# Kernel tuning notes

Hardware: AMD Instinct MI355X
Metric: run time of the kernel (lower is better)

The kernel has to match this reference:

```python
import jax, jax.numpy as jnp
import numpy as np

EMBED_DIM = 1024
HEADS = 16
D_HEAD = EMBED_DIM // HEADS
B, S = 2, 2048


def setup_inputs() -> dict:
    key = jax.random.key(0)
    ks = jax.random.split(key, 7)
    scale = 1.0 / np.sqrt(EMBED_DIM)
    inp = {
        "key": jax.random.normal(ks[0], (B, S, EMBED_DIM), dtype=jnp.float32),
        "query": jax.random.normal(ks[1], (B, S, EMBED_DIM), dtype=jnp.float32),
        "value": jax.random.normal(ks[2], (B, S, EMBED_DIM), dtype=jnp.float32),
        # causal mask, broadcastable to [B, H, Sq, Sk]
        "mask": jnp.tril(jnp.ones((S, S), dtype=bool))[None, None, :, :],
        # torch nn.Linear weights: [out_features, in_features], applied as x @ W.T
        "Wq": jax.random.normal(ks[3], (EMBED_DIM, EMBED_DIM), dtype=jnp.float32) * scale,
        "Wk": jax.random.normal(ks[4], (EMBED_DIM, EMBED_DIM), dtype=jnp.float32) * scale,
        "Wv": jax.random.normal(ks[5], (EMBED_DIM, EMBED_DIM), dtype=jnp.float32) * scale,
        "Wo": jax.random.normal(ks[6], (EMBED_DIM, EMBED_DIM), dtype=jnp.float32) * scale,
    }
    return inp


def reference(key, query, value, mask, Wq, Wk, Wv, Wo):
    b, sq, _ = query.shape
    sk = key.shape[1]
    # projections (torch Linear: x @ W.T), reshape to [B, H, S, Dh]
    q = (query @ Wq.T).reshape(b, sq, HEADS, D_HEAD).transpose(0, 2, 1, 3)
    k = (key @ Wk.T).reshape(b, sk, HEADS, D_HEAD).transpose(0, 2, 1, 3)
    v = (value @ Wv.T).reshape(b, sk, HEADS, D_HEAD).transpose(0, 2, 1, 3)
    # scaled dot-product scores [B, H, Sq, Sk]
    scores = jnp.einsum("bhqd,bhkd->bhqk", q, k) / jnp.sqrt(jnp.float32(D_HEAD))
    scores = jnp.where(mask, scores, jnp.float32(-1e9))
    attn = jax.nn.softmax(scores, axis=-1)
    # dropout p=0.0 -> identity
    out = jnp.einsum("bhqk,bhkd->bhqd", attn, v)  # [B, H, Sq, Dh]
    out = out.transpose(0, 2, 1, 3).reshape(b, sq, EMBED_DIM)
    return out @ Wo.T
```

## Files before the change

kernel.cpp:

```cpp
#include <hip/hip_runtime.h>
#include <stdint.h>


typedef unsigned short ushort_t;
typedef __attribute__((ext_vector_type(8))) __bf16 bf16x8;
typedef __attribute__((ext_vector_type(4))) float floatx4;

#define EMBED 1024
#define SEQ   2048
#define NH    16
#define DH    64
#define QK_SCALE 0.18033688011112042f

__device__ inline ushort_t f2b(float x) {
  unsigned u = __float_as_uint(x);
  u += 0x7FFFu + ((u >> 16) & 1u);
  return (ushort_t)(u >> 16);
}

__device__ inline unsigned pk2(float a, float b) {
  unsigned ua = __float_as_uint(a) + 0x8000u;
  unsigned ub = __float_as_uint(b) + 0x8000u;
  return __builtin_amdgcn_perm(ub, ua, 0x07060302u);
}

__device__ inline void gl_lds16(const ushort_t* g, ushort_t* l) {
  __builtin_amdgcn_global_load_lds(
      (const __attribute__((address_space(1))) unsigned int*)g,
      (__attribute__((address_space(3))) unsigned int*)l, 16, 0, 0);
}

struct CvtArgs {
  const float* src[16];
  ushort_t*    dst[16];
  float        scale[16];
};

__global__ __launch_bounds__(256) void cvt_kernel(CvtArgs a) {
  const int chunk = blockIdx.x >> 9;
  const int off = ((blockIdx.x & 511) << 11) + (threadIdx.x << 3);
  const float sc = a.scale[chunk];
  const float4* s = (const float4*)(a.src[chunk] + off);
  float4 f0 = s[0], f1 = s[1];
  union { ushort_t u[8]; uint4 v; } o;
  o.u[0] = f2b(f0.x * sc); o.u[1] = f2b(f0.y * sc);
  o.u[2] = f2b(f0.z * sc); o.u[3] = f2b(f0.w * sc);
  o.u[4] = f2b(f1.x * sc); o.u[5] = f2b(f1.y * sc);
  o.u[6] = f2b(f1.z * sc); o.u[7] = f2b(f1.w * sc);
  *(uint4*)(a.dst[chunk] + off) = o.v;
}

__device__ inline void store_sub(char* __restrict__ Cv, const int mode,
                                 const int ldc, const int row, const int col,
                                 const floatx4& acc) {
  if (mode == 0) {
    ushort_t* C = (ushort_t*)Cv;
#pragma unroll
    for (int r = 0; r < 4; ++r)
      C[(size_t)(row + r) * ldc + col] = f2b(acc[r]);
  } else if (mode == 1) {
    float* C = (float*)Cv;
#pragma unroll
    for (int r = 0; r < 4; ++r)
      C[(size_t)(row + r) * ldc + col] = acc[r];
  } else {
    ushort_t* C = (ushort_t*)Cv;
    const int b = row >> 11, s = row & 2047;
    const int h = col >> 6, d = col & 63;
    uint2 pk;
    pk.x = pk2(acc[0], acc[1]);
    pk.y = pk2(acc[2], acc[3]);
    *(uint2*)&C[(size_t)((b * NH + h) * DH + d) * SEQ + s] = pk;
  }
}

__device__ inline void gemm512_core(const ushort_t* __restrict__ A,
                                    const ushort_t* __restrict__ W,
                                    char* __restrict__ Cv, const int mode,
                                    const int ldc, const int m0, const int n0) {
  __shared__ ushort_t As[32 * 512];
  __shared__ ushort_t Bs[16 * 512];
  const int tid  = threadIdx.x;
  const int lane = tid & 63;
  const int wid  = tid >> 6;
  const int lm   = lane & 15;
  const int quad = lane >> 4;
  const int wm   = wid >> 1;
  const int wn   = wid & 1;

  floatx4 zero = {0.f, 0.f, 0.f, 0.f};
  floatx4 acc[4][4];
#pragma unroll
  for (int i = 0; i < 4; ++i)
#pragma unroll
    for (int j = 0; j < 4; ++j) acc[i][j] = zero;

  for (int k0 = 0; k0 < EMBED; k0 += 64) {
    __syncthreads();
#pragma unroll
    for (int u = 0; u < 6; ++u) {
      const int c   = wid * 6 + u;
      const int cb  = c & 31;
      const int sub = cb >> 1;
      const int kc  = (cb & 1) * 32 + quad * 8;
      if (c < 32)
        gl_lds16(A + (size_t)(m0 + sub * 16 + lm) * EMBED + k0 + kc, &As[cb * 512]);
      else
        gl_lds16(W + (size_t)(n0 + sub * 16 + lm) * EMBED + k0 + kc, &Bs[cb * 512]);
    }
    __syncthreads();

#pragma unroll
    for (int ks = 0; ks < 2; ++ks) {
      bf16x8 a[4], b[4];
#pragma unroll
      for (int i = 0; i < 4; ++i)
        a[i] = *(const bf16x8*)&As[((wm * 4 + i) * 2 + ks) * 512 + lane * 8];
#pragma unroll
      for (int j = 0; j < 4; ++j)
        b[j] = *(const bf16x8*)&Bs[((wn * 4 + j) * 2 + ks) * 512 + lane * 8];
#pragma unroll
      for (int i = 0; i < 4; ++i)
#pragma unroll
        for (int j = 0; j < 4; ++j)
          acc[i][j] = __builtin_amdgcn_mfma_f32_16x16x32_bf16(a[i], b[j], acc[i][j], 0, 0, 0);
    }
  }

#pragma unroll
  for (int i = 0; i < 4; ++i) {
    const int row = m0 + wm * 64 + i * 16 + quad * 4;
#pragma unroll
    for (int j = 0; j < 4; ++j)
      store_sub(Cv, mode, ldc, row, n0 + wn * 64 + j * 16 + lm, acc[i][j]);
  }
}

struct QkvArgs {
  const ushort_t* A[3];
  const ushort_t* W[3];
  char*           C[3];
};

__global__ __launch_bounds__(512, 4) void qkv_gemm(QkvArgs q) {
  const int z = blockIdx.z;
  gemm512_core(q.A[z], q.W[z], q.C[z], z == 2 ? 2 : 0, EMBED,
               blockIdx.x * 256, blockIdx.y * 128);
}

__global__ __launch_bounds__(256) void o_gemm(const ushort_t* __restrict__ A,
                                              const ushort_t* __restrict__ W,
                                              float* __restrict__ C) {
  __shared__ ushort_t As[16 * 512];
  __shared__ ushort_t Bs[16 * 512];
  const int m0 = blockIdx.x * 128, n0 = blockIdx.y * 128;
  const int tid  = threadIdx.x;
  const int lane = tid & 63;
  const int wid  = tid >> 6;
  const int lm   = lane & 15;
  const int quad = lane >> 4;

  floatx4 zero = {0.f, 0.f, 0.f, 0.f};
  floatx4 acc[4][4];
#pragma unroll
  for (int i = 0; i < 4; ++i)
#pragma unroll
    for (int j = 0; j < 4; ++j) acc[i][j] = zero;

  const int tm = (wid >> 1) * 4;
  const int tn = (wid & 1) * 4;

  for (int k0 = 0; k0 < EMBED; k0 += 64) {
    __syncthreads();
#pragma unroll
    for (int u = 0; u < 8; ++u) {
      const int c   = wid * 8 + u;
      const int cb  = c & 15;
      const int sub = cb >> 1;
      const int kc  = (cb & 1) * 32 + quad * 8;
      if (c < 16)
        gl_lds16(A + (size_t)(m0 + sub * 16 + lm) * EMBED + k0 + kc, &As[cb * 512]);
      else
        gl_lds16(W + (size_t)(n0 + sub * 16 + lm) * EMBED + k0 + kc, &Bs[cb * 512]);
    }
    __syncthreads();

#pragma unroll
    for (int ks = 0; ks < 2; ++ks) {
      bf16x8 a[4], b[4];
#pragma unroll
      for (int i = 0; i < 4; ++i)
        a[i] = *(const bf16x8*)&As[((tm + i) * 2 + ks) * 512 + lane * 8];
#pragma unroll
      for (int j = 0; j < 4; ++j)
        b[j] = *(const bf16x8*)&Bs[((tn + j) * 2 + ks) * 512 + lane * 8];
#pragma unroll
      for (int i = 0; i < 4; ++i)
#pragma unroll
        for (int j = 0; j < 4; ++j)
          acc[i][j] = __builtin_amdgcn_mfma_f32_16x16x32_bf16(a[i], b[j], acc[i][j], 0, 0, 0);
    }
  }

#pragma unroll
  for (int i = 0; i < 4; ++i) {
    const int row = m0 + (wid >> 1) * 64 + i * 16 + quad * 4;
#pragma unroll
    for (int j = 0; j < 4; ++j) {
      const int col = n0 + (wid & 1) * 64 + j * 16 + lm;
#pragma unroll
      for (int r = 0; r < 4; ++r)
        C[(size_t)(row + r) * EMBED + col] = acc[i][j][r];
    }
  }
}

__global__ __launch_bounds__(256) void attn_kernel(const ushort_t* __restrict__ Qp,
                                                   const ushort_t* __restrict__ Kp,
                                                   const ushort_t* __restrict__ VpT,
                                                   ushort_t* __restrict__ Ob) {
  __shared__ ushort_t Qs[16 * 512];
  __shared__ ushort_t Ks[8 * 512];
  __shared__ ushort_t VTs[8 * 512];
  __shared__ ushort_t Pw[4 * 2048];
  const int L = blockIdx.x;
  const int qb = 15 - (L >> 5);
  const int bh = L & 31;
  const int h = bh & (NH - 1), b = bh >> 4;
  const int tid = threadIdx.x, lane = tid & 63, wid = tid >> 6;
  const int lm = lane & 15, quad = lane >> 4;
  const size_t qkbase = ((size_t)b * SEQ) * EMBED + h * DH;
  const size_t vtbase = ((size_t)(b * NH + h)) * DH * SEQ;
  ushort_t* pwb = &Pw[wid * 2048];

#pragma unroll
  for (int u = 0; u < 4; ++u) {
    const int c = wid * 4 + u;
    gl_lds16(Qp + qkbase + (size_t)(qb * 128 + (c >> 1) * 16 + lm) * EMBED
                 + (c & 1) * 32 + quad * 8,
             &Qs[c * 512]);
  }
  asm volatile("s_waitcnt vmcnt(0)" ::: "memory");
  bf16x8 qf[2][2];
#pragma unroll
  for (int qg = 0; qg < 2; ++qg)
#pragma unroll
    for (int ks = 0; ks < 2; ++ks)
      qf[qg][ks] = *(const bf16x8*)&Qs[((wid * 2 + qg) * 2 + ks) * 512 + lane * 8];

  float l_part[2] = {0.f, 0.f};
  floatx4 zero = {0.f, 0.f, 0.f, 0.f};
  floatx4 o_acc[4][2];
#pragma unroll
  for (int d = 0; d < 4; ++d)
#pragma unroll
    for (int qg = 0; qg < 2; ++qg) o_acc[d][qg] = zero;

  const int kt_end = 2 * qb + 1;
  for (int kt = 0; kt <= kt_end; ++kt) {
    __syncthreads();
#pragma unroll
    for (int u = 0; u < 4; ++u) {
      const int t = wid * 4 + u;
      const int cb = t & 7;
      const int sub = cb >> 1;
      const int half = cb & 1;
      if (t < 8)
        gl_lds16(Kp + qkbase + (size_t)(kt * 64 + sub * 16 + lm) * EMBED
                     + half * 32 + quad * 8,
                 &Ks[cb * 512]);
      else
        gl_lds16(VpT + vtbase + (size_t)(sub * 16 + lm) * SEQ
                     + kt * 64 + half * 32 + quad * 8,
                 &VTs[cb * 512]);
    }
    __syncthreads();

    floatx4 s_acc[4][2];
#pragma unroll
    for (int i = 0; i < 4; ++i)
#pragma unroll
      for (int qg = 0; qg < 2; ++qg) s_acc[i][qg] = zero;
#pragma unroll
    for (int ks = 0; ks < 2; ++ks)
#pragma unroll
      for (int i = 0; i < 4; ++i) {
        bf16x8 kf = *(const bf16x8*)&Ks[(i * 2 + ks) * 512 + lane * 8];
#pragma unroll
        for (int qg = 0; qg < 2; ++qg)
          s_acc[i][qg] = __builtin_amdgcn_mfma_f32_16x16x32_bf16(kf, qf[qg][ks], s_acc[i][qg], 0, 0, 0);
      }

    const bool diag = (kt >= 2 * qb);
#pragma unroll
    for (int i = 0; i < 4; ++i) {
      const int s = i >> 1;
      const int quadB = ((i & 1) << 1) | (quad >> 1);
      const int gkk = kt * 64 + i * 16 + quad * 4;
#pragma unroll
      for (int qg = 0; qg < 2; ++qg) {
        float p[4];
#pragma unroll
        for (int r = 0; r < 4; ++r) p[r] = __builtin_amdgcn_exp2f(s_acc[i][qg][r]);
        if (diag) {
          const int gq = qb * 128 + wid * 32 + qg * 16 + lm;
#pragma unroll
          for (int r = 0; r < 4; ++r)
            if (gkk + r > gq) p[r] = 0.f;
        }
#pragma unroll
        for (int r = 0; r < 4; ++r) l_part[qg] += p[r];
        uint2 pk;
        pk.x = pk2(p[0], p[1]);
        pk.y = pk2(p[2], p[3]);
        *(uint2*)&pwb[(qg * 2 + s) * 512 + (quadB * 16 + lm) * 8 + ((quad & 1) << 2)] = pk;
      }
    }
    asm volatile("s_waitcnt lgkmcnt(0)" ::: "memory");

#pragma unroll
    for (int s = 0; s < 2; ++s) {
      bf16x8 pf[2];
#pragma unroll
      for (int qg = 0; qg < 2; ++qg)
        pf[qg] = *(const bf16x8*)&pwb[(qg * 2 + s) * 512 + lane * 8];
#pragma unroll
      for (int d = 0; d < 4; ++d) {
        bf16x8 vf = *(const bf16x8*)&VTs[(d * 2 + s) * 512 + lane * 8];
#pragma unroll
        for (int qg = 0; qg < 2; ++qg)
          o_acc[d][qg] = __builtin_amdgcn_mfma_f32_16x16x32_bf16(vf, pf[qg], o_acc[d][qg], 0, 0, 0);
      }
    }
  }

#pragma unroll
  for (int qg = 0; qg < 2; ++qg) {
    float l = l_part[qg];
    l += __shfl_xor(l, 16, 64);
    l += __shfl_xor(l, 32, 64);
    const float inv_l = 1.0f / l;
    const size_t orow = qkbase + (size_t)(qb * 128 + wid * 32 + qg * 16 + lm) * EMBED;
#pragma unroll
    for (int d = 0; d < 4; ++d) {
      uint2 pk;
      pk.x = pk2(o_acc[d][qg][0] * inv_l, o_acc[d][qg][1] * inv_l);
      pk.y = pk2(o_acc[d][qg][2] * inv_l, o_acc[d][qg][3] * inv_l);
      *(uint2*)&Ob[orow + d * 16 + quad * 4] = pk;
    }
  }
}

extern "C" void kernel_launch(void* const* d_in, const int* in_sizes, int n_in,
                              void* d_out, int out_size, void* d_ws, size_t ws_size,
                              hipStream_t stream) {
  const float* key   = (const float*)d_in[0];
  const float* query = (const float*)d_in[1];
  const float* value = (const float*)d_in[2];
  const float* Wq = (const float*)d_in[4];
  const float* Wk = (const float*)d_in[5];
  const float* Wv = (const float*)d_in[6];
  const float* Wo = (const float*)d_in[7];

  char* ws = (char*)d_ws;
  const size_t MB = 1024 * 1024;
  ushort_t* Xk  = (ushort_t*)(ws + 0 * MB);
  ushort_t* Xq  = (ushort_t*)(ws + 8 * MB);
  ushort_t* Xv  = (ushort_t*)(ws + 16 * MB);
  ushort_t* Wqb = (ushort_t*)(ws + 24 * MB);
  ushort_t* Wkb = (ushort_t*)(ws + 26 * MB);
  ushort_t* Wvb = (ushort_t*)(ws + 28 * MB);
  ushort_t* Wob = (ushort_t*)(ws + 30 * MB);
  ushort_t* Qp  = (ushort_t*)(ws + 32 * MB);
  ushort_t* Kp  = (ushort_t*)(ws + 40 * MB);
  ushort_t* VpT = (ushort_t*)(ws + 48 * MB);
  ushort_t* Ob  = (ushort_t*)(ws + 56 * MB);

  CvtArgs ca;
  const size_t CE = 1048576;
  for (int c = 0; c < 16; ++c) ca.scale[c] = 1.0f;
  for (int c = 0; c < 4; ++c) { ca.src[c]     = key   + c * CE; ca.dst[c]     = Xk + c * CE; }
  for (int c = 0; c < 4; ++c) { ca.src[4 + c] = query + c * CE; ca.dst[4 + c] = Xq + c * CE; }
  for (int c = 0; c < 4; ++c) { ca.src[8 + c] = value + c * CE; ca.dst[8 + c] = Xv + c * CE; }
  ca.src[12] = Wq; ca.dst[12] = Wqb; ca.scale[12] = QK_SCALE;
  ca.src[13] = Wk; ca.dst[13] = Wkb;
  ca.src[14] = Wv; ca.dst[14] = Wvb;
  ca.src[15] = Wo; ca.dst[15] = Wob;
  cvt_kernel<<<8192, 256, 0, stream>>>(ca);

  QkvArgs qa;
  qa.A[0] = Xq; qa.W[0] = Wqb; qa.C[0] = (char*)Qp;
  qa.A[1] = Xk; qa.W[1] = Wkb; qa.C[1] = (char*)Kp;
  qa.A[2] = Xv; qa.W[2] = Wvb; qa.C[2] = (char*)VpT;
  qkv_gemm<<<dim3(16, 8, 3), 512, 0, stream>>>(qa);

  attn_kernel<<<512, 256, 0, stream>>>(Qp, Kp, VpT, Ob);

  o_gemm<<<dim3(32, 8), 256, 0, stream>>>(Ob, Wob, (float*)d_out);
}
```

Baseline: 266.2 us.

## Double-buffer K/V tiles in attention and balance causal block ordering

The attention loop now keeps two LDS buffers for K and V^T and issues the next tile's async global-to-LDS loads before computing on the current tile, so load latency overlaps MFMA work. One of the two barriers per iteration goes away. The first tile is prefetched alongside Q. The block-to-query-tile mapping also changes so the second half of blocks visits query tiles in ascending order instead of descending, which alters how the uneven causal work is spread. LDS use per block grows, which may reduce occupancy.

```diff
diff --git a/kernel.cpp b/kernel.cpp
--- a/kernel.cpp
+++ b/kernel.cpp
@@ -220,11 +220,11 @@
                                                    const ushort_t* __restrict__ VpT,
                                                    ushort_t* __restrict__ Ob) {
   __shared__ ushort_t Qs[16 * 512];
-  __shared__ ushort_t Ks[8 * 512];
-  __shared__ ushort_t VTs[8 * 512];
+  __shared__ ushort_t Ks[2][8 * 512];
+  __shared__ ushort_t VTs[2][8 * 512];
   __shared__ ushort_t Pw[4 * 2048];
   const int L = blockIdx.x;
-  const int qb = 15 - (L >> 5);
+  const int qb = (L < 256) ? (15 - (L >> 5)) : ((L >> 5) - 8);
   const int bh = L & 31;
   const int h = bh & (NH - 1), b = bh >> 4;
   const int tid = threadIdx.x, lane = tid & 63, wid = tid >> 6;
@@ -240,7 +240,18 @@
                  + (c & 1) * 32 + quad * 8,
              &Qs[c * 512]);
   }
-  asm volatile("s_waitcnt vmcnt(0)" ::: "memory");
+#pragma unroll
+  for (int u = 0; u < 4; ++u) {
+    const int t = wid * 4 + u;
+    const int cb = t & 7, sub = cb >> 1, half = cb & 1;
+    if (t < 8)
+      gl_lds16(Kp + qkbase + (size_t)(sub * 16 + lm) * EMBED + half * 32 + quad * 8,
+               &Ks[0][cb * 512]);
+    else
+      gl_lds16(VpT + vtbase + (size_t)(sub * 16 + lm) * SEQ + half * 32 + quad * 8,
+               &VTs[0][cb * 512]);
+  }
+  asm volatile("s_waitcnt vmcnt(4)" ::: "memory");
   bf16x8 qf[2][2];
 #pragma unroll
   for (int qg = 0; qg < 2; ++qg)
@@ -258,23 +269,25 @@
 
   const int kt_end = 2 * qb + 1;
   for (int kt = 0; kt <= kt_end; ++kt) {
+    const int cur = kt & 1;
+    asm volatile("s_waitcnt vmcnt(0)" ::: "memory");
     __syncthreads();
-#pragma unroll
-    for (int u = 0; u < 4; ++u) {
-      const int t = wid * 4 + u;
-      const int cb = t & 7;
-      const int sub = cb >> 1;
-      const int half = cb & 1;
-      if (t < 8)
-        gl_lds16(Kp + qkbase + (size_t)(kt * 64 + sub * 16 + lm) * EMBED
-                     + half * 32 + quad * 8,
-                 &Ks[cb * 512]);
-      else
-        gl_lds16(VpT + vtbase + (size_t)(sub * 16 + lm) * SEQ
-                     + kt * 64 + half * 32 + quad * 8,
-                 &VTs[cb * 512]);
-    }
-    __syncthreads();
+    if (kt < kt_end) {
+      const int kn = kt + 1;
+#pragma unroll
+      for (int u = 0; u < 4; ++u) {
+        const int t = wid * 4 + u;
+        const int cb = t & 7, sub = cb >> 1, half = cb & 1;
+        if (t < 8)
+          gl_lds16(Kp + qkbase + (size_t)(kn * 64 + sub * 16 + lm) * EMBED
+                       + half * 32 + quad * 8,
+                   &Ks[cur ^ 1][cb * 512]);
+        else
+          gl_lds16(VpT + vtbase + (size_t)(sub * 16 + lm) * SEQ
+                       + kn * 64 + half * 32 + quad * 8,
+                   &VTs[cur ^ 1][cb * 512]);
+      }
+    }
 
     floatx4 s_acc[4][2];
 #pragma unroll
@@ -285,7 +298,7 @@
     for (int ks = 0; ks < 2; ++ks)
 #pragma unroll
       for (int i = 0; i < 4; ++i) {
-        bf16x8 kf = *(const bf16x8*)&Ks[(i * 2 + ks) * 512 + lane * 8];
+        bf16x8 kf = *(const bf16x8*)&Ks[cur][(i * 2 + ks) * 512 + lane * 8];
 #pragma unroll
         for (int qg = 0; qg < 2; ++qg)
           s_acc[i][qg] = __builtin_amdgcn_mfma_f32_16x16x32_bf16(kf, qf[qg][ks], s_acc[i][qg], 0, 0, 0);
@@ -326,7 +339,7 @@
         pf[qg] = *(const bf16x8*)&pwb[(qg * 2 + s) * 512 + lane * 8];
 #pragma unroll
       for (int d = 0; d < 4; ++d) {
-        bf16x8 vf = *(const bf16x8*)&VTs[(d * 2 + s) * 512 + lane * 8];
+        bf16x8 vf = *(const bf16x8*)&VTs[cur][(d * 2 + s) * 512 + lane * 8];
 #pragma unroll
         for (int qg = 0; qg < 2; ++qg)
           o_acc[d][qg] = __builtin_amdgcn_mfma_f32_16x16x32_bf16(vf, pf[qg], o_acc[d][qg], 0, 0, 0);
```

After: 254.7 us. 4.3% less time.
